# Performance work log

Measured on AMD Instinct MI355X. Metric: run time of the kernel, lower is better.

## Reference

```python
import jax, jax.numpy as jnp
import numpy as np

FEATURE_DIM = 768
NUM_HEADS = 16
HEAD_DIM = FEATURE_DIM // NUM_HEADS
SCALE = HEAD_DIM ** -0.5


def setup_inputs() -> dict:
    key = jax.random.key(0)
    ks = jax.random.split(key, 9)
    B, N, C = 4, 2048, FEATURE_DIM
    s = 0.02
    return {
        "x": jax.random.normal(ks[0], (B, N, C), dtype=jnp.float32),
        "wq": jax.random.normal(ks[1], (C, C), dtype=jnp.float32) * s,
        "bq": jax.random.normal(ks[2], (C,), dtype=jnp.float32) * s,
        "wk": jax.random.normal(ks[3], (C, C), dtype=jnp.float32) * s,
        "bk": jax.random.normal(ks[4], (C,), dtype=jnp.float32) * s,
        "wv": jax.random.normal(ks[5], (C, C), dtype=jnp.float32) * s,
        "bv": jax.random.normal(ks[6], (C,), dtype=jnp.float32) * s,
        "wo": jax.random.normal(ks[7], (C, C), dtype=jnp.float32) * s,
        "bo": jax.random.normal(ks[8], (C,), dtype=jnp.float32) * s,
    }


def reference(x, wq, bq, wk, bk, wv, bv, wo, bo):
    B, N, C = x.shape
    H, D = NUM_HEADS, HEAD_DIM
    # Linear layers use weight of shape (out, in): y = x @ W.T + b
    def proj(w, b):
        return (jnp.einsum("bnc,dc->bnd", x, w) + b).reshape(B, N, H, D).transpose(0, 2, 1, 3)
    q = proj(wq, bq)  # [B,H,N,D]
    k = proj(wk, bk)
    v = proj(wv, bv)
    attn = jnp.einsum("bhnd,bhmd->bhnm", q, k) * SCALE
    attn = jax.nn.softmax(attn, axis=-1)  # dropout = identity (eval mode)
    y = jnp.einsum("bhnm,bhmd->bhnd", attn, v).transpose(0, 2, 1, 3).reshape(B, N, C)
    y = y + x
    out = jnp.einsum("bnc,dc->bnd", y, wo) + bo
    out = out + y
    return out + x
```

## Files before the change

### kernel.cpp

```cpp
#include <hip/hip_runtime.h>
#include <hip/hip_bf16.h>

#define B_ 4
#define N_ 2048
#define C_ 768
#define H_ 16
#define D_ 48
#define SCALE_ 0.14433756729740643f
#define LOG2E_ 1.44269504088896f

using bf16 = __hip_bfloat16;
using bf16x8 = __attribute__((ext_vector_type(8))) short;
using f32x4  = __attribute__((ext_vector_type(4))) float;
using f32x16 = __attribute__((ext_vector_type(16))) float;
using u32x2  = __attribute__((ext_vector_type(2))) unsigned int;
using u32x4  = __attribute__((ext_vector_type(4))) unsigned int;

__device__ __forceinline__ unsigned short f2b(float f) {
  bf16 h = __float2bfloat16(f);
  return *reinterpret_cast<unsigned short*>(&h);
}
__device__ __forceinline__ unsigned int pack2(float lo, float hi) {
  return (unsigned int)f2b(lo) | ((unsigned int)f2b(hi) << 16);
}
__device__ __forceinline__ unsigned int pk2(float lo, float hi) {
  unsigned int r;
  asm("v_cvt_pk_bf16_f32 %0, %1, %2" : "=v"(r) : "v"(lo), "v"(hi));
  return r;
}
__device__ __forceinline__ uint4 ld8f_cvt(const float* p) {
  float4 a = *reinterpret_cast<const float4*>(p);
  float4 b = *reinterpret_cast<const float4*>(p + 4);
  uint4 u;
  u.x = pack2(a.x, a.y); u.y = pack2(a.z, a.w);
  u.z = pack2(b.x, b.y); u.w = pack2(b.z, b.w);
  return u;
}
__device__ __forceinline__ void gload_lds16(const bf16* g, bf16* l) {
  __builtin_amdgcn_global_load_lds(
      (const __attribute__((address_space(1))) unsigned int*)g,
      (__attribute__((address_space(3))) unsigned int*)l, 16, 0, 0);
}

__global__ __launch_bounds__(256) void cvt_bf16(
    const float* __restrict__ x,  const float* __restrict__ wq,
    const float* __restrict__ wk, const float* __restrict__ wv,
    const float* __restrict__ wo,
    bf16* __restrict__ xb, bf16* __restrict__ wqkvb, bf16* __restrict__ wob)
{
  const int job = blockIdx.y;
  const float* src; bf16* dst; int n;
  if (job == 0)      { src = x;  dst = xb;              n = B_ * N_ * C_; }
  else if (job == 1) { src = wq; dst = wqkvb;           n = C_ * C_; }
  else if (job == 2) { src = wk; dst = wqkvb + C_ * C_; n = C_ * C_; }
  else if (job == 3) { src = wv; dst = wqkvb + 2 * C_ * C_; n = C_ * C_; }
  else               { src = wo; dst = wob;             n = C_ * C_; }
  const int stride = gridDim.x * 256 * 8;
  for (int i = (blockIdx.x * 256 + threadIdx.x) * 8; i < n; i += stride)
    *(uint4*)(dst + i) = ld8f_cvt(src + i);
}

__global__ __launch_bounds__(256) void gemm_qkv(
    const bf16* __restrict__ A, const bf16* __restrict__ Bw,
    const float* __restrict__ bq, const float* __restrict__ bk,
    const float* __restrict__ bv,
    bf16* __restrict__ Q, bf16* __restrict__ K, bf16* __restrict__ V)
{
  __shared__ __align__(16) bf16 As[128 * 64];
  __shared__ __align__(16) bf16 Bs[128 * 64];

  const int tid  = threadIdx.x;
  const int lane = tid & 63, wid = tid >> 6;
  const int wm = (wid >> 1) * 64, wn = (wid & 1) * 64;
  const int row0 = blockIdx.y * 128, col0 = blockIdx.x * 128;
  const int mb = lane & 15, g4 = lane >> 4;
  const int srow = lane >> 3;
  const int schunk = (lane & 7) ^ (srow & 7);

  f32x4 acc[4][4];
#pragma unroll
  for (int i = 0; i < 4; ++i)
#pragma unroll
    for (int j = 0; j < 4; ++j) acc[i][j] = (f32x4){0.f, 0.f, 0.f, 0.f};

  for (int k0 = 0; k0 < C_; k0 += 64) {
#pragma unroll
    for (int t = 0; t < 4; ++t) {
      const int rt = wid * 32 + t * 8;
      gload_lds16(A  + (size_t)(row0 + rt + srow) * C_ + k0 + schunk * 8,
                  As + rt * 64);
      gload_lds16(Bw + (size_t)(col0 + rt + srow) * C_ + k0 + schunk * 8,
                  Bs + rt * 64);
    }
    __syncthreads();
#pragma unroll
    for (int ks = 0; ks < 2; ++ks) {
      const int kchunk = ks * 4 + g4;
      bf16x8 af[4], bfr[4];
#pragma unroll
      for (int i = 0; i < 4; ++i) {
        const int row = wm + i * 16 + mb;
        af[i] = *(const bf16x8*)(As + row * 64 + (kchunk ^ (row & 7)) * 8);
      }
#pragma unroll
      for (int j = 0; j < 4; ++j) {
        const int col = wn + j * 16 + mb;
        bfr[j] = *(const bf16x8*)(Bs + col * 64 + (kchunk ^ (col & 7)) * 8);
      }
#pragma unroll
      for (int i = 0; i < 4; ++i)
#pragma unroll
        for (int j = 0; j < 4; ++j)
          acc[i][j] = __builtin_amdgcn_mfma_f32_16x16x32_bf16(af[i], bfr[j], acc[i][j], 0, 0, 0);
    }
    __syncthreads();
  }

  const int z = blockIdx.x / 6;
  const float* bias = (z == 0) ? bq : (z == 1) ? bk : bv;
  bf16* dst = (z == 0) ? Q : (z == 1) ? K : V;
  const float sc = (z == 0) ? (SCALE_ * LOG2E_) : 1.0f;
  const int crow = g4 * 4;
#pragma unroll
  for (int j = 0; j < 4; ++j) {
    const int oo = col0 - z * 768 + wn + j * 16 + mb;
    const int h = oo / D_, d = oo % D_;
    const float bb = bias[oo];
#pragma unroll
    for (int i = 0; i < 4; ++i) {
#pragma unroll
      for (int reg = 0; reg < 4; ++reg) {
        const int r = row0 + wm + i * 16 + crow + reg;
        const int b_ = r >> 11, n = r & (N_ - 1);
        dst[(((size_t)(b_ * H_ + h)) * N_ + n) * D_ + d] =
            __float2bfloat16((acc[i][j][reg] + bb) * sc);
      }
    }
  }
}

__global__ __launch_bounds__(256) void qkv_reshape(
    bf16* __restrict__ Q, bf16* __restrict__ K,
    const bf16* __restrict__ Vtmp, bf16* __restrict__ Vf)
{
  __shared__ short T[64 * 50];
  const int bh = blockIdx.x;
  const int t0 = blockIdx.y * 64;
  const int tid = threadIdx.x;
  const size_t base = (size_t)bh * (N_ * D_) + (size_t)t0 * D_;
#pragma unroll 1
  for (int wbuf = 0; wbuf < 2; ++wbuf) {
    bf16* P = (wbuf ? K : Q) + base;
    for (int cc = tid; cc < 384; cc += 256) {
      const int r = cc / 6, ch = cc % 6;
      bf16x8 v8 = *(const bf16x8*)(P + r * D_ + ch * 8);
#pragma unroll
      for (int e = 0; e < 8; ++e) T[r * 50 + ch * 8 + e] = v8[e];
    }
    __syncthreads();
    for (int w = tid; w < 384; w += 256) {
      const int sub = w / 192, rem = w % 192;
      const int kc = rem / 64, rem2 = rem % 64;
      const int g2 = rem2 >> 5, m5 = rem2 & 31;
      bf16x8 o;
#pragma unroll
      for (int e = 0; e < 8; ++e)
        o[e] = T[(sub * 32 + m5) * 50 + kc * 16 + g2 * 8 + e];
      *(bf16x8*)(P + w * 8) = o;
    }
    __syncthreads();
  }
  {
    const bf16* Pv = Vtmp + base;
    for (int cc = tid; cc < 384; cc += 256) {
      const int r = cc / 6, ch = cc % 6;
      bf16x8 v8 = *(const bf16x8*)(Pv + r * D_ + ch * 8);
#pragma unroll
      for (int e = 0; e < 8; ++e) T[r * 50 + ch * 8 + e] = v8[e];
    }
    __syncthreads();
    bf16* W = Vf + (size_t)bh * (N_ * 64) + (size_t)t0 * 64;
    for (int w = tid; w < 512; w += 256) {
      const int ksl = w >> 7;
      const int dt  = (w >> 6) & 1;
      const int l   = w & 63;
      const int hi = l >> 5, m5 = l & 31;
      bf16x8 o;
      if (dt == 0) {
#pragma unroll
        for (int e = 0; e < 8; ++e)
          o[e] = T[(ksl * 16 + hi * 8 + e) * 50 + m5];
      } else if (m5 < 16) {
#pragma unroll
        for (int e = 0; e < 8; ++e)
          o[e] = T[(ksl * 16 + hi * 8 + e) * 50 + 32 + m5];
      } else {
        const short fill = (m5 == 16) ? (short)0x3F80 : (short)0;
#pragma unroll
        for (int e = 0; e < 8; ++e) o[e] = fill;
      }
      *(bf16x8*)(W + (size_t)(((ksl * 2 + dt) * 64 + l) * 8)) = o;
    }
  }
}

__global__ __launch_bounds__(256) void attn_mfma(
    const bf16* __restrict__ Qf, const bf16* __restrict__ Kf,
    const bf16* __restrict__ Vf, const float* __restrict__ x,
    bf16* __restrict__ Yb)
{
  const int tid  = threadIdx.x;
  const int lane = tid & 63, wid = tid >> 6;
  const int m5 = lane & 31, hi = lane >> 5;
  const int bh = blockIdx.x;
  const int b_ = bh >> 4, h = bh & 15;
  const int q0 = blockIdx.y * 128 + wid * 32;
  const size_t slab  = (size_t)bh * (N_ * D_);
  const size_t slabV = (size_t)bh * (N_ * 64);

  bf16x8 qf[3];
  const int kgq = q0 >> 5;
#pragma unroll
  for (int kc = 0; kc < 3; ++kc)
    qf[kc] = *(const bf16x8*)(Qf + slab + (size_t)(((kgq * 3 + kc) * 64) + lane) * 8);

  f32x16 Oacc[2];
#pragma unroll
  for (int dt = 0; dt < 2; ++dt)
#pragma unroll
    for (int r = 0; r < 16; ++r) Oacc[dt][r] = 0.f;

  bf16x8 kf[2][2][3];
  auto loadK = [&](int kk0, int p) {
    const int kg = kk0 >> 5;
#pragma unroll
    for (int mt = 0; mt < 2; ++mt)
#pragma unroll
      for (int kc = 0; kc < 3; ++kc)
        kf[p][mt][kc] = *(const bf16x8*)(Kf + slab +
            (size_t)((((kg + mt) * 3 + kc) * 64) + lane) * 8);
  };
  auto body = [&](int k0c, int p) {
    const int kg16 = k0c >> 4;
    bf16x8 vA[4][2];
#pragma unroll
    for (int ks = 0; ks < 4; ++ks)
#pragma unroll
      for (int dt = 0; dt < 2; ++dt)
        vA[ks][dt] = *(const bf16x8*)(Vf + slabV +
            (size_t)((((kg16 + ks) * 2 + dt) * 64) + lane) * 8);
    f32x16 st[2];
#pragma unroll
    for (int mt = 0; mt < 2; ++mt) {
      f32x16 z;
#pragma unroll
      for (int r = 0; r < 16; ++r) z[r] = 0.f;
      st[mt] = __builtin_amdgcn_mfma_f32_32x32x16_bf16(kf[p][mt][0], qf[0], z, 0, 0, 0);
      st[mt] = __builtin_amdgcn_mfma_f32_32x32x16_bf16(kf[p][mt][1], qf[1], st[mt], 0, 0, 0);
      st[mt] = __builtin_amdgcn_mfma_f32_32x32x16_bf16(kf[p][mt][2], qf[2], st[mt], 0, 0, 0);
    }
#pragma unroll
    for (int mt = 0; mt < 2; ++mt)
#pragma unroll
      for (int r = 0; r < 16; ++r)
        st[mt][r] = __builtin_amdgcn_exp2f(st[mt][r]);
#pragma unroll
    for (int ks = 0; ks < 4; ++ks) {
      const f32x16& S = st[ks >> 1];
      const int qa = (ks & 1) * 2;
      const unsigned A0 = pk2(S[4 * qa + 0], S[4 * qa + 1]);
      const unsigned A1 = pk2(S[4 * qa + 2], S[4 * qa + 3]);
      const unsigned B0 = pk2(S[4 * qa + 4], S[4 * qa + 5]);
      const unsigned B1 = pk2(S[4 * qa + 6], S[4 * qa + 7]);
      const u32x2 r02 = __builtin_amdgcn_permlane32_swap(A0, B0, false, false);
      const u32x2 r13 = __builtin_amdgcn_permlane32_swap(A1, B1, false, false);
      u32x4 pw;
      pw.x = r02.x; pw.y = r13.x; pw.z = r02.y; pw.w = r13.y;
      const bf16x8 pb = (bf16x8)pw;
      Oacc[0] = __builtin_amdgcn_mfma_f32_32x32x16_bf16(vA[ks][0], pb, Oacc[0], 0, 0, 0);
      Oacc[1] = __builtin_amdgcn_mfma_f32_32x32x16_bf16(vA[ks][1], pb, Oacc[1], 0, 0, 0);
    }
  };

  loadK(0, 0);
  for (int k0 = 0; k0 < N_; k0 += 128) {
    loadK(k0 + 64, 1);
    body(k0, 0);
    if (k0 + 128 < N_) loadK(k0 + 128, 0);
    body(k0 + 64, 1);
  }

  const float lf = Oacc[1][8];
  const unsigned lu = __builtin_bit_cast(unsigned, lf);
  const u32x2 lsw = __builtin_amdgcn_permlane32_swap(lu, lu, false, false);
  const float Lv = __builtin_bit_cast(float, lsw.x);
  const float inv = 1.f / Lv;

  const int n = q0 + m5;
  const size_t rowoff = ((size_t)(b_ * N_ + n)) * C_ + h * D_;
#pragma unroll
  for (int qq = 0; qq < 4; ++qq) {
    const size_t off = rowoff + 8 * qq + 4 * hi;
    const float4 xr = *(const float4*)(x + off);
    u32x2 wv;
    wv.x = pk2(Oacc[0][4 * qq + 0] * inv + xr.x, Oacc[0][4 * qq + 1] * inv + xr.y);
    wv.y = pk2(Oacc[0][4 * qq + 2] * inv + xr.z, Oacc[0][4 * qq + 3] * inv + xr.w);
    *(u32x2*)(Yb + off) = wv;
  }
#pragma unroll
  for (int qq = 0; qq < 2; ++qq) {
    const size_t off = rowoff + 32 + 8 * qq + 4 * hi;
    const float4 xr = *(const float4*)(x + off);
    u32x2 wv;
    wv.x = pk2(Oacc[1][4 * qq + 0] * inv + xr.x, Oacc[1][4 * qq + 1] * inv + xr.y);
    wv.y = pk2(Oacc[1][4 * qq + 2] * inv + xr.z, Oacc[1][4 * qq + 3] * inv + xr.w);
    *(u32x2*)(Yb + off) = wv;
  }
}

__global__ __launch_bounds__(256) void gemm_out(
    const bf16* __restrict__ Yb, const bf16* __restrict__ Bw,
    const float* __restrict__ bo, const float* __restrict__ x,
    float* __restrict__ out)
{
  __shared__ __align__(16) bf16 As[128 * 64];
  __shared__ __align__(16) bf16 Bs[128 * 64];

  const int tid  = threadIdx.x;
  const int lane = tid & 63, wid = tid >> 6;
  const int wm = (wid >> 1) * 64, wn = (wid & 1) * 64;
  const int row0 = blockIdx.y * 128, col0 = blockIdx.x * 128;
  const int mb = lane & 15, g4 = lane >> 4;
  const int srow = lane >> 3;
  const int schunk = (lane & 7) ^ (srow & 7);

  f32x4 acc[4][4];
#pragma unroll
  for (int i = 0; i < 4; ++i)
#pragma unroll
    for (int j = 0; j < 4; ++j) acc[i][j] = (f32x4){0.f, 0.f, 0.f, 0.f};

  for (int k0 = 0; k0 < C_; k0 += 64) {
#pragma unroll
    for (int t = 0; t < 4; ++t) {
      const int rt = wid * 32 + t * 8;
      gload_lds16(Yb + (size_t)(row0 + rt + srow) * C_ + k0 + schunk * 8,
                  As + rt * 64);
      gload_lds16(Bw + (size_t)(col0 + rt + srow) * C_ + k0 + schunk * 8,
                  Bs + rt * 64);
    }
    __syncthreads();
#pragma unroll
    for (int ks = 0; ks < 2; ++ks) {
      const int kchunk = ks * 4 + g4;
      bf16x8 af[4], bfr[4];
#pragma unroll
      for (int i = 0; i < 4; ++i) {
        const int row = wm + i * 16 + mb;
        af[i] = *(const bf16x8*)(As + row * 64 + (kchunk ^ (row & 7)) * 8);
      }
#pragma unroll
      for (int j = 0; j < 4; ++j) {
        const int col = wn + j * 16 + mb;
        bfr[j] = *(const bf16x8*)(Bs + col * 64 + (kchunk ^ (col & 7)) * 8);
      }
#pragma unroll
      for (int i = 0; i < 4; ++i)
#pragma unroll
        for (int j = 0; j < 4; ++j)
          acc[i][j] = __builtin_amdgcn_mfma_f32_16x16x32_bf16(af[i], bfr[j], acc[i][j], 0, 0, 0);
    }
    __syncthreads();
  }

  const int crow = g4 * 4;
#pragma unroll
  for (int j = 0; j < 4; ++j) {
    const int o = col0 + wn + j * 16 + mb;
    const float bb = bo[o];
#pragma unroll
    for (int i = 0; i < 4; ++i) {
#pragma unroll
      for (int reg = 0; reg < 4; ++reg) {
        const int r = row0 + wm + i * 16 + crow + reg;
        const size_t off = (size_t)r * C_ + o;
        out[off] = acc[i][j][reg] + bb + __bfloat162float(Yb[off]) + x[off];
      }
    }
  }
}

extern "C" void kernel_launch(void* const* d_in, const int* in_sizes, int n_in,
                              void* d_out, int out_size, void* d_ws, size_t ws_size,
                              hipStream_t stream)
{
  const float* x  = (const float*)d_in[0];
  const float* wq = (const float*)d_in[1];
  const float* bq = (const float*)d_in[2];
  const float* wk = (const float*)d_in[3];
  const float* bk = (const float*)d_in[4];
  const float* wv = (const float*)d_in[5];
  const float* bv = (const float*)d_in[6];
  const float* wo = (const float*)d_in[7];
  const float* bo = (const float*)d_in[8];
  float* out = (float*)d_out;

  const size_t nEl  = (size_t)B_ * N_ * C_;
  const size_t wEl  = (size_t)C_ * C_;
  const size_t vfEl = (size_t)B_ * H_ * N_ * 64;
  bf16* Q     = (bf16*)d_ws;
  bf16* K     = Q + nEl;
  bf16* Vf    = K + nEl;
  bf16* Yb    = Vf + vfEl;
  bf16* xb    = Yb + nEl;
  bf16* wqkvb = xb + nEl;
  bf16* wob   = wqkvb + 3 * wEl;

  dim3 gcvt(768, 5);
  cvt_bf16<<<gcvt, dim3(256), 0, stream>>>(x, wq, wk, wv, wo, xb, wqkvb, wob);

  dim3 gqkv(18, 64);
  gemm_qkv<<<gqkv, dim3(256), 0, stream>>>(xb, wqkvb, bq, bk, bv, Q, K, Yb);

  dim3 grs(B_ * H_, N_ / 64);
  qkv_reshape<<<grs, dim3(256), 0, stream>>>(Q, K, Yb, Vf);

  dim3 gattn(B_ * H_, N_ / 128);
  attn_mfma<<<gattn, dim3(256), 0, stream>>>(Q, K, Vf, x, Yb);

  dim3 gout(6, 64);
  gemm_out<<<gout, dim3(256), 0, stream>>>(Yb, wob, bo, x, out);
}
```

Baseline: 267.5 us.

## Software-pipeline attention loop so next QK MFMA overlaps current softmax and PV

```diff
diff --git a/kernel.cpp b/kernel.cpp
--- a/kernel.cpp
+++ b/kernel.cpp
@@ -224,50 +224,46 @@
   for (int kc = 0; kc < 3; ++kc)
     qf[kc] = *(const bf16x8*)(Qf + slab + (size_t)(((kgq * 3 + kc) * 64) + lane) * 8);
 
+  f32x16 zf;
+#pragma unroll
+  for (int r = 0; r < 16; ++r) zf[r] = 0.f;
+
   f32x16 Oacc[2];
 #pragma unroll
   for (int dt = 0; dt < 2; ++dt)
 #pragma unroll
     for (int r = 0; r < 16; ++r) Oacc[dt][r] = 0.f;
 
-  bf16x8 kf[2][2][3];
-  auto loadK = [&](int kk0, int p) {
-    const int kg = kk0 >> 5;
-#pragma unroll
-    for (int mt = 0; mt < 2; ++mt)
-#pragma unroll
-      for (int kc = 0; kc < 3; ++kc)
-        kf[p][mt][kc] = *(const bf16x8*)(Kf + slab +
-            (size_t)((((kg + mt) * 3 + kc) * 64) + lane) * 8);
+  const bf16* Kp = Kf + slab  + (size_t)lane * 8;
+  const bf16* Vp = Vf + slabV + (size_t)lane * 8;
+
+  bf16x8 kf[2][3];
+  auto loadK = [&](int t, int p) {
+    const bf16* kp = Kp + (size_t)t * (3 * 512);
+#pragma unroll
+    for (int kc = 0; kc < 3; ++kc)
+      kf[p][kc] = *(const bf16x8*)(kp + kc * 512);
   };
-  auto body = [&](int k0c, int p) {
-    const int kg16 = k0c >> 4;
-    bf16x8 vA[4][2];
-#pragma unroll
-    for (int ks = 0; ks < 4; ++ks)
+  auto vload = [&](int t, bf16x8 (&vA)[2][2]) {
+    const bf16* vp = Vp + (size_t)t * 2048;
+#pragma unroll
+    for (int ks = 0; ks < 2; ++ks)
 #pragma unroll
       for (int dt = 0; dt < 2; ++dt)
-        vA[ks][dt] = *(const bf16x8*)(Vf + slabV +
-            (size_t)((((kg16 + ks) * 2 + dt) * 64) + lane) * 8);
-    f32x16 st[2];
-#pragma unroll
-    for (int mt = 0; mt < 2; ++mt) {
-      f32x16 z;
-#pragma unroll
-      for (int r = 0; r < 16; ++r) z[r] = 0.f;
-      st[mt] = __builtin_amdgcn_mfma_f32_32x32x16_bf16(kf[p][mt][0], qf[0], z, 0, 0, 0);
-      st[mt] = __builtin_amdgcn_mfma_f32_32x32x16_bf16(kf[p][mt][1], qf[1], st[mt], 0, 0, 0);
-      st[mt] = __builtin_amdgcn_mfma_f32_32x32x16_bf16(kf[p][mt][2], qf[2], st[mt], 0, 0, 0);
-    }
-#pragma unroll
-    for (int mt = 0; mt < 2; ++mt)
-#pragma unroll
-      for (int r = 0; r < 16; ++r)
-        st[mt][r] = __builtin_amdgcn_exp2f(st[mt][r]);
-#pragma unroll
-    for (int ks = 0; ks < 4; ++ks) {
-      const f32x16& S = st[ks >> 1];
-      const int qa = (ks & 1) * 2;
+        vA[ks][dt] = *(const bf16x8*)(vp + (ks * 2 + dt) * 512);
+  };
+  auto qk = [&](int p, f32x16& dst) {
+    dst = __builtin_amdgcn_mfma_f32_32x32x16_bf16(kf[p][0], qf[0], zf, 0, 0, 0);
+    dst = __builtin_amdgcn_mfma_f32_32x32x16_bf16(kf[p][1], qf[1], dst, 0, 0, 0);
+    dst = __builtin_amdgcn_mfma_f32_32x32x16_bf16(kf[p][2], qf[2], dst, 0, 0, 0);
+  };
+  auto smpv = [&](f32x16& S, bf16x8 (&vA)[2][2]) {
+#pragma unroll
+    for (int r = 0; r < 16; ++r)
+      S[r] = __builtin_amdgcn_exp2f(S[r]);
+#pragma unroll
+    for (int ks = 0; ks < 2; ++ks) {
+      const int qa = ks * 2;
       const unsigned A0 = pk2(S[4 * qa + 0], S[4 * qa + 1]);
       const unsigned A1 = pk2(S[4 * qa + 2], S[4 * qa + 3]);
       const unsigned B0 = pk2(S[4 * qa + 4], S[4 * qa + 5]);
@@ -282,12 +278,24 @@
     }
   };
 
+  f32x16 stA, stB;
+  bf16x8 vA0[2][2], vA1[2][2];
   loadK(0, 0);
-  for (int k0 = 0; k0 < N_; k0 += 128) {
-    loadK(k0 + 64, 1);
-    body(k0, 0);
-    if (k0 + 128 < N_) loadK(k0 + 128, 0);
-    body(k0 + 64, 1);
+  loadK(1, 1);
+  qk(0, stA);
+  loadK(2, 0);
+
+#pragma unroll 1
+  for (int it = 0; it < 32; ++it) {
+    const int t = it * 2;
+    vload(t, vA0);
+    qk(1, stB);
+    loadK(t + 3, 1);
+    smpv(stA, vA0);
+    vload(t + 1, vA1);
+    qk(0, stA);
+    loadK(t + 4, 0);
+    smpv(stB, vA1);
   }
 
   const float lf = Oacc[1][8];
```

After: 273.6 us. 2.3% more time.
